# Kernel optimization log

Hardware: AMD Instinct MI355X
Metric: run time of the kernel (lower is better)

## Reference

```python
import jax, jax.numpy as jnp
import numpy as np

NEG = -1e30  # log-domain "zero" (safe in fp32/bf16 logaddexp)
EPS = 1e-7   # keras backend epsilon used by K.ctc_batch_cost


def setup_inputs() -> dict:
    key = jax.random.key(0)
    k1, k2 = jax.random.split(key)
    B, T, C, L = 64, 1024, 512, 128
    y_pred = jax.random.uniform(k1, (B, T, C), dtype=jnp.float32)
    y_true = jax.random.randint(k2, (B, L), 0, C - 1)  # blank = C-1 excluded
    return {"y_true": y_true, "y_pred": y_pred}


def ctc_batch_cost(y_true, y_pred):
    """Faithful jax port of keras.backend.ctc_batch_cost with full-length
    labels/inputs (as the CTCLayer passes input_length=T, label_length=L
    for every batch element). Returns per-example loss of shape [B, 1].

    K.ctc_batch_cost computes log(y_pred + eps) and feeds it to
    tf.nn.ctc_loss, which applies an internal softmax; we replicate that
    with log_softmax(log(y_pred + eps)). blank index = C - 1.
    """
    B, T, C = y_pred.shape
    L = y_true.shape[1]
    blank = C - 1
    logp = jax.nn.log_softmax(jnp.log(y_pred + EPS), axis=-1)  # [B,T,C]

    # Extended label sequence with interleaved blanks: length S = 2L+1
    S = 2 * L + 1
    ext = jnp.full((B, S), blank, dtype=y_true.dtype).at[:, 1::2].set(y_true)
    ext_m2 = jnp.concatenate(
        [jnp.full((B, 2), -1, dtype=ext.dtype), ext[:, :-2]], axis=1)
    # alpha[s-2] -> alpha[s] skip allowed iff ext[s] != blank and ext[s] != ext[s-2]
    skip = (ext != blank) & (ext != ext_m2)  # [B,S]

    # Emission log-probs gathered along the extended sequence: [B,T,S]
    emit = jnp.take_along_axis(
        logp, jnp.broadcast_to(ext[:, None, :], (B, T, S)), axis=2)

    # alpha_0: only states 0 (blank) and 1 (first label) are reachable
    alpha0 = (jnp.full((B, S), NEG, dtype=logp.dtype)
              .at[:, 0].set(emit[:, 0, 0])
              .at[:, 1].set(emit[:, 0, 1]))

    neg1 = jnp.full((B, 1), NEG, dtype=logp.dtype)
    neg2 = jnp.full((B, 2), NEG, dtype=logp.dtype)

    def step(alpha, emit_t):
        a1 = jnp.concatenate([neg1, alpha[:, :-1]], axis=1)   # stay->next
        a2 = jnp.concatenate([neg2, alpha[:, :-2]], axis=1)   # skip blank
        a2 = jnp.where(skip, a2, NEG)
        comb = jnp.logaddexp(jnp.logaddexp(alpha, a1), a2)
        return comb + emit_t, None

    emit_tm = jnp.transpose(emit, (1, 0, 2))  # time-major [T,B,S]
    alphaT, _ = jax.lax.scan(step, alpha0, emit_tm[1:])

    # p(labels) = alpha_T[S-1] + alpha_T[S-2]
    loss = -jnp.logaddexp(alphaT[:, -1], alphaT[:, -2])  # [B]
    return loss[:, None]


def reference(y_true, y_pred):
    return ctc_batch_cost(y_true, y_pred)
```

## Files before the change

kernel.cpp:

```cpp
#include <hip/hip_runtime.h>


#define EPSF 1e-7f
static constexpr int NB = 64;
static constexpr int NT = 1024;
static constexpr int NC = 512;
static constexpr int NL = 128;
static constexpr int CHUNK = 16;
static constexpr int NCH = NT / CHUNK;

typedef unsigned int uint32;

__device__ __forceinline__ unsigned short rn_bf16(float x) {
    uint32 b = __float_as_uint(x);
    return (unsigned short)((b + 0x7FFFu + ((b >> 16) & 1u)) >> 16);
}

__global__ __launch_bounds__(256) void ctc_prep(const float* __restrict__ Y,
                                                const int* __restrict__ y_true,
                                                uint32* __restrict__ qlab,
                                                float* __restrict__ eblank,
                                                int mode) {
    int gtid = blockIdx.x * 256 + threadIdx.x;
    int w = gtid >> 6;
    int lane = gtid & 63;
    int b = w >> 10;
    const float* row = Y + (size_t)w * NC;

    float4 v0 = *reinterpret_cast<const float4*>(row + lane * 4);
    float4 v1 = *reinterpret_cast<const float4*>(row + (NC / 2) + lane * 4);
    float s = ((v0.x + v0.y) + (v0.z + v0.w)) + ((v1.x + v1.y) + (v1.z + v1.w));
#pragma unroll
    for (int d = 1; d < 64; d <<= 1) s += __shfl_xor(s, d);

    if (mode == 1) {
        float rb = row[NC - 1] + EPSF;
        float inv = 1.0f / (s + NC * EPSF);
        float rbi = 1.0f / rb;
        int2 lp = *reinterpret_cast<const int2*>(y_true + b * NL + lane * 2);
        float qx = (row[lp.x] + EPSF) * rbi;
        float qy = (row[lp.y] + EPSF) * rbi;
        uint32 pk = (uint32)rn_bf16(qx) | ((uint32)rn_bf16(qy) << 16);
        qlab[(size_t)w * (NL / 2) + lane] = pk;
        if (lane == 0) eblank[w] = rb * inv;
    } else {
        if (lane == 0) eblank[w] = 256.0f / (s + NC * EPSF);
    }
}

__device__ __forceinline__ float dpp_wave_shr1(float x) {
    return __int_as_float(__builtin_amdgcn_update_dpp(
        0, __float_as_int(x), 0x138, 0xF, 0xF, true));
}

__device__ __forceinline__ float dpp_wave_max(float m) {
#define DPPMAX_(ctrl)                                                     \
    m = fmaxf(m, __int_as_float(__builtin_amdgcn_update_dpp(              \
                     0, __float_as_int(m), ctrl, 0xF, 0xF, true)))
    DPPMAX_(0x111); DPPMAX_(0x112); DPPMAX_(0x114); DPPMAX_(0x118);
    DPPMAX_(0x142); DPPMAX_(0x143);
#undef DPPMAX_
    return __int_as_float(
        __builtin_amdgcn_readlane(__float_as_int(m), 63));
}

__device__ __forceinline__ float dpp_wave_sum63(float v) {
#define DPPADD_(ctrl)                                                     \
    v += __int_as_float(__builtin_amdgcn_update_dpp(                      \
        0, __float_as_int(v), ctrl, 0xF, 0xF, true))
    DPPADD_(0x111); DPPADD_(0x112); DPPADD_(0x114); DPPADD_(0x118);
    DPPADD_(0x142); DPPADD_(0x143);
#undef DPPADD_
    return v;
}

__global__ __launch_bounds__(64) void ctc_rec1(const uint32* __restrict__ A,
                                               const float* __restrict__ Bv,
                                               const int* __restrict__ y_true,
                                               float* __restrict__ out) {
    const int b = blockIdx.x;
    const int l = threadIdx.x;
    const int* lab = y_true + b * NL;

    int lab_m1 = (l == 0) ? -1 : lab[2 * l - 1];
    int lab0 = lab[2 * l];
    int lab1 = lab[2 * l + 1];
    float sk0 = (lab0 != lab_m1) ? 1.0f : 0.0f;
    float sk1 = (lab1 != lab0) ? 1.0f : 0.0f;

    float slog = 0.0f;
#pragma unroll
    for (int k = 0; k < NT / 64; k++)
        slog += logf(Bv[b * NT + k * 64 + l]);
    float sred = dpp_wave_sum63(slog);

    float p0 = (l == 0) ? 1.0f : 0.0f;
    float p1 = 0.0f, p2 = 0.0f, p3 = 0.0f, pS = 0.0f;
    int ksum = 0;

    uint32 L0[CHUNK], L1[CHUNK], L2[CHUNK], L3[CHUNK];

    auto load = [&](int c, uint32(&L)[CHUNK]) {
        const uint32* base = A + ((size_t)b * NT + c * CHUNK) * (NL / 2) + l;
#pragma unroll
        for (int j = 0; j < CHUNK; j++) L[j] = base[(size_t)j * (NL / 2)];
    };

    auto process = [&](uint32(&L)[CHUNK]) {
#pragma unroll
        for (int j = 0; j < CHUNK; j++) {
            float qx = __uint_as_float(L[j] << 16);
            float qy = __uint_as_float(L[j] & 0xFFFF0000u);
            float s3 = dpp_wave_shr1(p3);
            float n0 = p0 + s3;
            float n1 = (p1 + p0 + sk0 * s3) * qx;
            float n2 = p2 + p1;
            float n3 = (p3 + p2 + sk1 * p1) * qy;
            pS = pS + p3;
            p0 = n0; p1 = n1; p2 = n2; p3 = n3;
        }
        float m = fmaxf(fmaxf(p0, p1), fmaxf(p2, p3));
        m = fmaxf(m, (l == 63) ? pS : 0.0f);
        float mall = fmaxf(dpp_wave_max(m), 1e-30f);
        int e = (int)(__float_as_uint(mall) >> 23) - 127;
        float sc = __uint_as_float((uint32)(127 - e) << 23);
        p0 *= sc; p1 *= sc; p2 *= sc; p3 *= sc; pS *= sc;
        ksum += e;
    };

    load(0, L0);
    load(1, L1);
    load(2, L2);
    for (int c = 0; c < NCH; c += 4) {
        if (c + 3 < NCH) load(c + 3, L3);
        process(L0);
        if (c + 4 < NCH) load(c + 4, L0);
        process(L1);
        if (c + 5 < NCH) load(c + 5, L1);
        process(L2);
        if (c + 6 < NCH) load(c + 6, L2);
        process(L3);
    }

    if (l == 63) {
        float tot = p3 + pS;
        out[b] = -(logf(tot) + (float)ksum * 0.69314718055994531f + sred);
    }
}

__global__ __launch_bounds__(64) void ctc_rec0(const float* __restrict__ A,
                                               const float* __restrict__ Bv,
                                               const int* __restrict__ y_true,
                                               float* __restrict__ out) {
    const int b = blockIdx.x;
    const int l = threadIdx.x;
    const int* lab = y_true + b * NL;

    int lab_m1 = (l == 0) ? -1 : lab[2 * l - 1];
    int lab0 = lab[2 * l];
    int lab1 = lab[2 * l + 1];
    float sk0 = (lab0 != lab_m1) ? 1.0f : 0.0f;
    float sk1 = (lab1 != lab0) ? 1.0f : 0.0f;

    float p0 = (l == 0) ? 1.0f : 0.0f;
    float p1 = 0.0f, p2 = 0.0f, p3 = 0.0f, pS = 0.0f;
    int ksum = 0;

    for (int t = 0; t < NT; t++) {
        const float* base = A + ((size_t)b * NT + t) * NC;
        float iv = Bv[b * NT + t];
        float eb = (base[NC - 1] + EPSF) * iv;
        float ex = (base[lab0] + EPSF) * iv;
        float ey = (base[lab1] + EPSF) * iv;
        float s3 = dpp_wave_shr1(p3);
        float n0 = (p0 + s3) * eb;
        float n1 = (p1 + p0 + sk0 * s3) * ex;
        float n2 = (p2 + p1) * eb;
        float n3 = (p3 + p2 + sk1 * p1) * ey;
        pS = (pS + p3) * eb;
        p0 = n0; p1 = n1; p2 = n2; p3 = n3;
        if ((t & 15) == 15) {
            float m = fmaxf(fmaxf(p0, p1), fmaxf(p2, p3));
            m = fmaxf(m, (l == 63) ? pS : 0.0f);
            float mall = fmaxf(dpp_wave_max(m), 1e-30f);
            int e = (int)(__float_as_uint(mall) >> 23) - 127;
            float sc = __uint_as_float((uint32)(127 - e) << 23);
            p0 *= sc; p1 *= sc; p2 *= sc; p3 *= sc; pS *= sc;
            ksum += e;
        }
    }

    if (l == 63) {
        float tot = p3 + pS;
        out[b] = -(logf(tot) +
                   (float)(ksum - 8192) * 0.69314718055994531f);
    }
}

extern "C" void kernel_launch(void* const* d_in, const int* in_sizes, int n_in,
                              void* d_out, int out_size, void* d_ws, size_t ws_size,
                              hipStream_t stream) {
    const int* y_true = (const int*)d_in[0];
    const float* y_pred = (const float*)d_in[1];
    float* out = (float*)d_out;

    const size_t qlab_bytes = (size_t)NB * NT * (NL / 2) * sizeof(uint32);
    const size_t eb_bytes = (size_t)NB * NT * sizeof(float);

    if (ws_size >= qlab_bytes + eb_bytes) {
        uint32* qlab = (uint32*)d_ws;
        float* eblank = (float*)((char*)d_ws + qlab_bytes);
        ctc_prep<<<NB * NT / 4, 256, 0, stream>>>(y_pred, y_true, qlab, eblank, 1);
        ctc_rec1<<<NB, 64, 0, stream>>>(qlab, eblank, y_true, out);
    } else {
        float* invb = (float*)d_ws;
        ctc_prep<<<NB * NT / 4, 256, 0, stream>>>(y_pred, y_true, nullptr, invb, 0);
        ctc_rec0<<<NB, 64, 0, stream>>>(y_pred, invb, y_true, out);
    }
}
```

Measured before the change: 65.80 us.

## Pack eight batch waves per block and load 64-step chunks before compute

The recurrence kernel now runs eight batch elements as eight waves in one 512-thread block instead of one wave per block. The rotating four-buffer prefetch is replaced by loading a 64-step chunk into registers and then processing it, with scheduling barriers between the phases. Renormalization still happens every 16 steps inside the chunk. This aims to simplify scheduling and let co-resident waves hide load latency. It risks fewer CUs being used, waves sharing SIMDs, and exposed load latency at each chunk boundary.

```diff
diff --git a/kernel.cpp b/kernel.cpp
--- a/kernel.cpp
+++ b/kernel.cpp
@@ -6,7 +6,7 @@
 static constexpr int NT = 1024;
 static constexpr int NC = 512;
 static constexpr int NL = 128;
-static constexpr int CHUNK = 16;
+static constexpr int CHUNK = 64;
 static constexpr int NCH = NT / CHUNK;
 
 typedef unsigned int uint32;
@@ -74,12 +74,13 @@
     return v;
 }
 
-__global__ __launch_bounds__(64) void ctc_rec1(const uint32* __restrict__ A,
-                                               const float* __restrict__ Bv,
-                                               const int* __restrict__ y_true,
-                                               float* __restrict__ out) {
-    const int b = blockIdx.x;
-    const int l = threadIdx.x;
+__global__ __launch_bounds__(512) void ctc_rec1(const uint32* __restrict__ A,
+                                                const float* __restrict__ Bv,
+                                                const int* __restrict__ y_true,
+                                                float* __restrict__ out) {
+    const int wid = threadIdx.x >> 6;
+    const int b = blockIdx.x * 8 + wid;
+    const int l = threadIdx.x & 63;
     const int* lab = y_true + b * NL;
 
     int lab_m1 = (l == 0) ? -1 : lab[2 * l - 1];
@@ -98,15 +99,14 @@
     float p1 = 0.0f, p2 = 0.0f, p3 = 0.0f, pS = 0.0f;
     int ksum = 0;
 
-    uint32 L0[CHUNK], L1[CHUNK], L2[CHUNK], L3[CHUNK];
-
-    auto load = [&](int c, uint32(&L)[CHUNK]) {
+    uint32 L[CHUNK];
+
+    for (int c = 0; c < NCH; ++c) {
         const uint32* base = A + ((size_t)b * NT + c * CHUNK) * (NL / 2) + l;
 #pragma unroll
         for (int j = 0; j < CHUNK; j++) L[j] = base[(size_t)j * (NL / 2)];
-    };
-
-    auto process = [&](uint32(&L)[CHUNK]) {
+        __builtin_amdgcn_sched_barrier(0);
+
 #pragma unroll
         for (int j = 0; j < CHUNK; j++) {
             float qx = __uint_as_float(L[j] << 16);
@@ -118,28 +118,18 @@
             float n3 = (p3 + p2 + sk1 * p1) * qy;
             pS = pS + p3;
             p0 = n0; p1 = n1; p2 = n2; p3 = n3;
+
+            if ((j & 15) == 15) {
+                float m = fmaxf(fmaxf(p0, p1), fmaxf(p2, p3));
+                m = fmaxf(m, (l == 63) ? pS : 0.0f);
+                float mall = fmaxf(dpp_wave_max(m), 1e-30f);
+                int e = (int)(__float_as_uint(mall) >> 23) - 127;
+                float sc = __uint_as_float((uint32)(127 - e) << 23);
+                p0 *= sc; p1 *= sc; p2 *= sc; p3 *= sc; pS *= sc;
+                ksum += e;
+            }
         }
-        float m = fmaxf(fmaxf(p0, p1), fmaxf(p2, p3));
-        m = fmaxf(m, (l == 63) ? pS : 0.0f);
-        float mall = fmaxf(dpp_wave_max(m), 1e-30f);
-        int e = (int)(__float_as_uint(mall) >> 23) - 127;
-        float sc = __uint_as_float((uint32)(127 - e) << 23);
-        p0 *= sc; p1 *= sc; p2 *= sc; p3 *= sc; pS *= sc;
-        ksum += e;
-    };
-
-    load(0, L0);
-    load(1, L1);
-    load(2, L2);
-    for (int c = 0; c < NCH; c += 4) {
-        if (c + 3 < NCH) load(c + 3, L3);
-        process(L0);
-        if (c + 4 < NCH) load(c + 4, L0);
-        process(L1);
-        if (c + 5 < NCH) load(c + 5, L1);
-        process(L2);
-        if (c + 6 < NCH) load(c + 6, L2);
-        process(L3);
+        __builtin_amdgcn_sched_barrier(0);
     }
 
     if (l == 63) {
@@ -211,7 +201,7 @@
         uint32* qlab = (uint32*)d_ws;
         float* eblank = (float*)((char*)d_ws + qlab_bytes);
         ctc_prep<<<NB * NT / 4, 256, 0, stream>>>(y_pred, y_true, qlab, eblank, 1);
-        ctc_rec1<<<NB, 64, 0, stream>>>(qlab, eblank, y_true, out);
+        ctc_rec1<<<NB / 8, 512, 0, stream>>>(qlab, eblank, y_true, out);
     } else {
         float* invb = (float*)d_ws;
         ctc_prep<<<NB * NT / 4, 256, 0, stream>>>(y_pred, y_true, nullptr, invb, 0);
```

Measured after the change: 84.74 us. 1.29x slower.
